# Optimization experiments

Measured on AMD Instinct MI355X. Metric: run time of the kernel, lower is better.

The kernel has to match this reference:

```python
import jax, jax.numpy as jnp
import numpy as np

B, S, D = 2, 2048, 2048
H, KV, HD = 32, 8, 64  # num_heads, num_kv_heads, head_dim
NREP = H // KV


def rotate_half(x):
    x1, x2 = x[..., : x.shape[-1] // 2], x[..., x.shape[-1] // 2 :]
    return jnp.concatenate((-x2, x1), axis=-1)


def setup_inputs() -> dict:
    key = jax.random.key(0)
    ks = jax.random.split(key, 5)
    x = jax.random.normal(ks[0], (B, S, D), dtype=jnp.float32)
    # weights stored as [in, out] so y = x @ W (same math as nn.Linear with random init)
    Wq = jax.random.normal(ks[1], (D, D), dtype=jnp.float32) * (D ** -0.5)
    Wk = jax.random.normal(ks[2], (D, KV * HD), dtype=jnp.float32) * (D ** -0.5)
    Wv = jax.random.normal(ks[3], (D, KV * HD), dtype=jnp.float32) * (D ** -0.5)
    Wo = jax.random.normal(ks[4], (D, D), dtype=jnp.float32) * (D ** -0.5)
    # standard RoPE tables, broadcastable over [B, H, S, HD]
    inv_freq = 1.0 / (10000.0 ** (jnp.arange(0, HD, 2, dtype=jnp.float32) / HD))
    freqs = jnp.arange(S, dtype=jnp.float32)[:, None] * inv_freq[None, :]  # [S, HD/2]
    emb = jnp.concatenate((freqs, freqs), axis=-1)  # [S, HD]
    cos = jnp.cos(emb)[None, None]  # [1,1,S,HD]
    sin = jnp.sin(emb)[None, None]
    # causal mask, masked where == 0
    attention_mask = jnp.tril(jnp.ones((S, S), dtype=jnp.int32))[None, None]
    return {"x": x, "cos": cos, "sin": sin, "Wq": Wq, "Wk": Wk, "Wv": Wv,
            "Wo": Wo, "attention_mask": attention_mask}


def reference(x, cos, sin, Wq, Wk, Wv, Wo, attention_mask):
    b, s, _ = x.shape
    q = (x @ Wq).reshape(b, s, H, HD).transpose(0, 2, 1, 3)   # [B,H,S,HD]
    k = (x @ Wk).reshape(b, s, KV, HD).transpose(0, 2, 1, 3)  # [B,KV,S,HD]
    v = (x @ Wv).reshape(b, s, KV, HD).transpose(0, 2, 1, 3)  # [B,KV,S,HD]
    # RoPE (elementwise) commutes with head-repeat; apply before grouping
    q = q * cos + rotate_half(q) * sin
    k = k * cos + rotate_half(k) * sin
    # GQA head broadcast instead of repeat_interleave: group q as [B,KV,NREP,S,HD]
    qg = q.reshape(b, KV, NREP, s, HD)
    scores = jnp.einsum('bgrqd,bgkd->bgrqk', qg, k) / jnp.sqrt(jnp.float32(HD))
    scores = jnp.where(attention_mask[:, :, None] == 0, jnp.float32(-1e9), scores)
    probs = jax.nn.softmax(scores, axis=-1)
    out = jnp.einsum('bgrqk,bgkd->bgrqd', probs, v)           # [B,KV,NREP,S,HD]
    out = out.reshape(b, H, s, HD).transpose(0, 2, 1, 3).reshape(b, s, H * HD)
    return out @ Wo
```

## Files before the change

### kernel.cpp

```cpp
#include <hip/hip_runtime.h>
#include <hip/hip_bf16.h>
#include <stdint.h>

#define B_ 2
#define S_ 2048
#define D_ 2048
#define H_ 32
#define KV_ 8
#define HD_ 64
#define NQKV 3072

typedef __bf16 bf16_t;
typedef __bf16 bf16x8 __attribute__((ext_vector_type(8)));
typedef __bf16 bf16x4 __attribute__((ext_vector_type(4)));
typedef float  f32x4  __attribute__((ext_vector_type(4)));
typedef float  f32x16 __attribute__((ext_vector_type(16)));
typedef unsigned int u32;
typedef u32 u32x4 __attribute__((ext_vector_type(4)));

typedef const __attribute__((address_space(1))) uint32_t* gp1_t;
typedef __attribute__((address_space(3))) uint32_t* lp3_t;

__device__ inline void gload_lds16(const void* g, void* l) {
  __builtin_amdgcn_global_load_lds((gp1_t)(uintptr_t)g, (lp3_t)(uint32_t)(uintptr_t)l,
                                   16, 0, 0);
}

__device__ inline u32 pkbf(float a, float b) {
  union { bf16_t h[2]; u32 u; } v;
  v.h[0] = (bf16_t)a; v.h[1] = (bf16_t)b;
  return v.u;
}

__device__ inline void pl32swap(u32 &a, u32 &b) {
  asm("v_permlane32_swap_b32 %0, %1" : "+v"(a), "+v"(b));
}

__global__ void cvt_f32_bf16(const float* __restrict__ in, bf16_t* __restrict__ out, int n4) {
  int i = blockIdx.x * blockDim.x + threadIdx.x;
  if (i < n4) {
    float4 v = ((const float4*)in)[i];
    bf16x4 o;
    o[0] = (bf16_t)v.x; o[1] = (bf16_t)v.y; o[2] = (bf16_t)v.z; o[3] = (bf16_t)v.w;
    ((bf16x4*)out)[i] = o;
  }
}

__global__ void transpose_cvt(const float* __restrict__ in, bf16_t* __restrict__ out,
                              int C, int row_off) {
  __shared__ float t[32][33];
  int tx = threadIdx.x, ty = threadIdx.y;
  int c0 = blockIdx.x * 32, r0 = blockIdx.y * 32;
#pragma unroll
  for (int j = 0; j < 4; ++j)
    t[ty + j*8][tx] = in[(int64_t)(r0 + ty + j*8) * C + c0 + tx];
  __syncthreads();
#pragma unroll
  for (int j = 0; j < 4; ++j)
    out[(int64_t)(row_off + c0 + ty + j*8) * 2048 + r0 + tx] = (bf16_t)t[tx][ty + j*8];
}

__global__ void v_transpose(const bf16_t* __restrict__ Vbuf, bf16_t* __restrict__ Vt) {
  __shared__ bf16_t t[32][34];
  const int tx = threadIdx.x, ty = threadIdx.y;
  const int c0 = blockIdx.x * 32;
  const int s0 = blockIdx.y * 32;
  const int b  = blockIdx.z;
#pragma unroll
  for (int j = 0; j < 4; ++j)
    t[ty + j*8][tx] = Vbuf[(int64_t)(b * S_ + s0 + ty + j*8) * 512 + c0 + tx];
  __syncthreads();
#pragma unroll
  for (int j = 0; j < 4; ++j)
    Vt[(int64_t)(b * 512 + c0 + ty + j*8) * S_ + s0 + tx] = t[tx][ty + j*8];
}

#define QSCALE 0.18033688011112042f
template <int BN, int EPI>
__global__ __launch_bounds__(512, 2) void gemm256(const bf16_t* __restrict__ A,
                                                  const bf16_t* __restrict__ Bt,
                                                  const float* __restrict__ cosb,
                                                  const float* __restrict__ sinb,
                                                  bf16_t* __restrict__ Q,
                                                  bf16_t* __restrict__ Kr,
                                                  bf16_t* __restrict__ Vbuf,
                                                  float* __restrict__ Cout,
                                                  int N, int K) {
  constexpr int NB = BN / 64;
  constexpr int LT = 4 + NB;
  constexpr int WCOLS = BN / 4;
  constexpr int NF = WCOLS / 16;

  __shared__ bf16_t As[2][256 * 64];
  __shared__ bf16_t Bs[2][BN * 64];

  const int tid = threadIdx.x;
  const int w = tid >> 6, lane = tid & 63;
  const int l15 = lane & 15, l4 = lane >> 4;
  const int wr = w >> 2, wc = w & 3;
  const int bm = blockIdx.y * 256, bn = blockIdx.x * BN;

  const int rw = w * 8 + (lane >> 3);
  const int srcg = ((lane & 7) ^ ((lane >> 3) & 7)) << 3;
  const bf16_t* PA[4];
  const bf16_t* PB[NB];
#pragma unroll
  for (int L = 0; L < 4; ++L)
    PA[L] = A + (int64_t)(bm + L * 64 + rw) * K + srcg;
#pragma unroll
  for (int L = 0; L < NB; ++L)
    PB[L] = Bt + (int64_t)(bn + L * 64 + rw) * K + srcg;

  const int NK = K >> 6;
  const int xr = l15 & 7;
  const int g0 = (l4 ^ xr) << 3;
  const int g1 = ((4 + l4) ^ xr) << 3;

  f32x4 acc[8][NF] = {};

#pragma unroll
  for (int s = 0; s < LT; ++s) {
    if (s < 4) gload_lds16(PA[s], &As[0][s * 4096 + w * 512]);
    else       gload_lds16(PB[s - 4], &Bs[0][(s - 4) * 4096 + w * 512]);
  }
  asm volatile("s_waitcnt vmcnt(0)" ::: "memory");
  __syncthreads();

  for (int t = 0; t < NK; ++t) {
    const int p = t & 1;
    const bool more = (t + 1) < NK;
    const int toff = (t + 1) << 6;
    const bf16_t* Ab = &As[p][0];
    const bf16_t* Bb = &Bs[p][0];

    bf16x8 ball[NF][2];
#pragma unroll
    for (int nn = 0; nn < NF; ++nn) {
      const int rb = wc * WCOLS + nn * 16 + l15;
      ball[nn][0] = *(const bf16x8*)(Bb + rb * 64 + g0);
      ball[nn][1] = *(const bf16x8*)(Bb + rb * 64 + g1);
    }

#pragma unroll
    for (int mh = 0; mh < 2; ++mh) {
      if (more) {
        const int s0 = mh * (LT / 2), s1 = s0 + LT / 2;
#pragma unroll
        for (int s = s0; s < s1; ++s) {
          if (s < 4) gload_lds16(PA[s] + toff, &As[p ^ 1][s * 4096 + w * 512]);
          else       gload_lds16(PB[s - 4] + toff, &Bs[p ^ 1][(s - 4) * 4096 + w * 512]);
        }
      }
      bf16x8 af[4][2];
#pragma unroll
      for (int mm = 0; mm < 4; ++mm) {
        const int ra = wr * 128 + (mh * 4 + mm) * 16 + l15;
        af[mm][0] = *(const bf16x8*)(Ab + ra * 64 + g0);
        af[mm][1] = *(const bf16x8*)(Ab + ra * 64 + g1);
      }
      __builtin_amdgcn_s_setprio(1);
#pragma unroll
      for (int mm = 0; mm < 4; ++mm)
#pragma unroll
        for (int nn = 0; nn < NF; ++nn) {
          acc[mh*4+mm][nn] = __builtin_amdgcn_mfma_f32_16x16x32_bf16(
              af[mm][0], ball[nn][0], acc[mh*4+mm][nn], 0, 0, 0);
          acc[mh*4+mm][nn] = __builtin_amdgcn_mfma_f32_16x16x32_bf16(
              af[mm][1], ball[nn][1], acc[mh*4+mm][nn], 0, 0, 0);
        }
      __builtin_amdgcn_s_setprio(0);
    }
    if (more) {
      asm volatile("s_waitcnt vmcnt(0)" ::: "memory");
      __syncthreads();
    }
  }

  if constexpr (EPI == 0) {
#pragma unroll
    for (int m = 0; m < 8; ++m) {
      const int row = bm + wr * 128 + m * 16 + l4 * 4;
#pragma unroll
      for (int n = 0; n < NF; ++n) {
        const int col = bn + wc * WCOLS + n * 16 + l15;
#pragma unroll
        for (int r = 0; r < 4; ++r)
          Cout[(int64_t)(row + r) * N + col] = acc[m][n][r];
      }
    }
  } else {
    const int colbase = bn + wc * 64;
    if (colbase < 2048) {
      const int h = colbase >> 6;
#pragma unroll
      for (int m = 0; m < 8; ++m) {
#pragma unroll
        for (int r = 0; r < 4; ++r) {
          const int srow = bm + wr * 128 + m * 16 + l4 * 4 + r;
          const int b = srow >> 11, s = srow & 2047;
          const float* cs = cosb + s * HD_;
          const float* sn = sinb + s * HD_;
          bf16_t* qp = Q + ((int64_t)(b * H_ + h) * S_ + s) * HD_;
#pragma unroll
          for (int n = 0; n < 4; ++n) {
            const int d = n * 16 + l15;
            const float sgn = (n & 2) ? 1.f : -1.f;
            float o = (acc[m][n][r] * cs[d] + sgn * acc[m][n ^ 2][r] * sn[d]) * QSCALE;
            qp[d] = (bf16_t)o;
          }
        }
      }
    } else if (colbase < 2560) {
      const int kvh = (colbase - 2048) >> 6;
#pragma unroll
      for (int m = 0; m < 8; ++m) {
#pragma unroll
        for (int r = 0; r < 4; ++r) {
          const int srow = bm + wr * 128 + m * 16 + l4 * 4 + r;
          const int b = srow >> 11, s = srow & 2047;
          const float* cs = cosb + s * HD_;
          const float* sn = sinb + s * HD_;
          bf16_t* kp = Kr + ((int64_t)(b * KV_ + kvh) * S_ + s) * HD_;
#pragma unroll
          for (int n = 0; n < 4; ++n) {
            const int d = n * 16 + l15;
            const float sgn = (n & 2) ? 1.f : -1.f;
            float o = acc[m][n][r] * cs[d] + sgn * acc[m][n ^ 2][r] * sn[d];
            kp[d] = (bf16_t)o;
          }
        }
      }
    } else {
      const int ccb = colbase - 2560;
#pragma unroll
      for (int m = 0; m < 8; ++m) {
#pragma unroll
        for (int r = 0; r < 4; ++r) {
          const int srow = bm + wr * 128 + m * 16 + l4 * 4 + r;
          bf16_t* vp = Vbuf + (int64_t)srow * 512 + ccb;
#pragma unroll
          for (int n = 0; n < 4; ++n)
            vp[n * 16 + l15] = (bf16_t)acc[m][n][r];
        }
      }
    }
  }
}

#define SHIFT_ 8.0f
__global__ __launch_bounds__(256, 2) void attn7(const bf16_t* __restrict__ Q,
                                                const bf16_t* __restrict__ Kr,
                                                const bf16_t* __restrict__ Vt,
                                                bf16_t* __restrict__ AO) {
  const int bk = blockIdx.x;
  const int b = bk >> 3, kvh = bk & 7;
  const int y = blockIdx.y;
  const int q0A = y * 32, q0B = (63 - y) * 32;
  const int tid = threadIdx.x;
  const int w = tid >> 6, lane = tid & 63;
  const int l31 = lane & 31, hi = lane >> 5;
  const int h = kvh * 4 + w;

  __shared__ __align__(16) bf16_t Ks[3][64 * 64];
  __shared__ __align__(16) bf16_t Vs[3][64 * 64];

  const bf16_t* Kg = Kr + (int64_t)(b * KV_ + kvh) * S_ * HD_;
  const bf16_t* Vg = Vt + (int64_t)(b * KV_ + kvh) * HD_ * S_;

  const int rL = (w << 3) + (lane >> 3);
  const int sgr = ((lane & 7) ^ (rL & 7)) << 3;
  const bf16_t* Ksrc = Kg + (int64_t)rL * HD_ + sgr;
  const bf16_t* Vsrc = Vg + (int64_t)rL * S_ + sgr;

  const int NT = (63 - y) / 2 + 1;

  auto stage = [&](int t) {
    const int tc = (t < NT) ? t : (NT - 1);
    char* Kd = (char*)Ks + (t % 3) * 8192 + w * 1024;
    char* Vd = (char*)Vs + (t % 3) * 8192 + w * 1024;
    gload_lds16(Ksrc + (int64_t)tc * 64 * HD_, Kd);
    gload_lds16(Ksrc + (int64_t)(tc * 64 + 32) * HD_, Kd + 4096);
    gload_lds16(Vsrc + tc * 64, Vd);
    gload_lds16(Vsrc + (int64_t)32 * S_ + tc * 64, Vd + 4096);
  };

  const bf16_t* QbA = Q + ((int64_t)(b * H_ + h) * S_ + q0A) * HD_;
  const bf16_t* QbB = Q + ((int64_t)(b * H_ + h) * S_ + q0B) * HD_;
  bf16x8 qfA[4], qfB[4];
#pragma unroll
  for (int ds = 0; ds < 4; ++ds) {
    qfA[ds] = *(const bf16x8*)(QbA + l31 * HD_ + ds * 16 + hi * 8);
    qfB[ds] = *(const bf16x8*)(QbB + l31 * HD_ + ds * 16 + hi * 8);
  }

  f32x16 aA0 = {}, aA1 = {}, aB0 = {}, aB1 = {};
  float lhA = 0.f, lhB = 0.f;
  const int xorb = l31 & 7;

  const f32x16 sinit = {-SHIFT_, -SHIFT_, -SHIFT_, -SHIFT_,
                        -SHIFT_, -SHIFT_, -SHIFT_, -SHIFT_,
                        -SHIFT_, -SHIFT_, -SHIFT_, -SHIFT_,
                        -SHIFT_, -SHIFT_, -SHIFT_, -SHIFT_};

  auto softmax_pack = [&](const f32x16 &sacc, bool diag, float &lh,
                          bf16x8 &pf0, bf16x8 &pf1) {
    float p[16];
#pragma unroll
    for (int r = 0; r < 16; ++r) {
      float sc = sacc[r];
      if (diag) {
        int kvpos = (r & 3) + 8 * (r >> 2) + 4 * hi;
        if (kvpos > l31) sc = -1e30f;
      }
      p[r] = __builtin_amdgcn_exp2f(sc);
    }
    float t0 = (p[0] + p[1]) + (p[2] + p[3]);
    float t1 = (p[4] + p[5]) + (p[6] + p[7]);
    float t2 = (p[8] + p[9]) + (p[10] + p[11]);
    float t3 = (p[12] + p[13]) + (p[14] + p[15]);
    lh += (t0 + t1) + (t2 + t3);
    u32 pk[8];
#pragma unroll
    for (int i = 0; i < 8; ++i) pk[i] = pkbf(p[2*i], p[2*i+1]);
    u32 a0 = pk[0], b0 = pk[2]; pl32swap(a0, b0);
    u32 a1 = pk[1], b1 = pk[3]; pl32swap(a1, b1);
    u32 a2 = pk[4], b2 = pk[6]; pl32swap(a2, b2);
    u32 a3 = pk[5], b3 = pk[7]; pl32swap(a3, b3);
    pf0 = __builtin_bit_cast(bf16x8, (u32x4){a0, a1, b0, b1});
    pf1 = __builtin_bit_cast(bf16x8, (u32x4){a2, a3, b2, b3});
  };

  stage(0);
  stage(1);

  for (int t = 0; t < NT; ++t) {
    asm volatile("s_waitcnt vmcnt(4)" ::: "memory");
    __syncthreads();
    stage(t + 2);
    const char* KsB = (const char*)Ks + (t % 3) * 8192;
    const char* VsB = (const char*)Vs + (t % 3) * 8192;
#pragma unroll
    for (int sub = 0; sub < 2; ++sub) {
      const int kvbase = t * 64 + sub * 32;
      if (kvbase <= q0B) {
        const bool actA = (kvbase <= q0A);
        const char* Kbase = KsB + (sub * 32 + l31) * 128;
        bf16x8 kf[4];
#pragma unroll
        for (int ds = 0; ds < 4; ++ds)
          kf[ds] = *(const bf16x8*)(Kbase + ((((ds << 1) + hi) ^ xorb) << 4));
        f32x16 sA = sinit, sB = sinit;
        __builtin_amdgcn_s_setprio(1);
#pragma unroll
        for (int ds = 0; ds < 4; ++ds)
          sB = __builtin_amdgcn_mfma_f32_32x32x16_bf16(kf[ds], qfB[ds], sB, 0, 0, 0);
        if (actA) {
#pragma unroll
          for (int ds = 0; ds < 4; ++ds)
            sA = __builtin_amdgcn_mfma_f32_32x32x16_bf16(kf[ds], qfA[ds], sA, 0, 0, 0);
        }
        __builtin_amdgcn_s_setprio(0);
        bf16x8 pA0, pA1, pB0, pB1;
        softmax_pack(sB, kvbase == q0B, lhB, pB0, pB1);
        if (actA) softmax_pack(sA, kvbase == q0A, lhA, pA0, pA1);
        const char* Vb0 = VsB + l31 * 128;
        const char* Vb1 = VsB + (32 + l31) * 128;
        const int c0 = (sub << 2) + hi;
        const int c1 = c0 + 2;
        bf16x8 v00 = *(const bf16x8*)(Vb0 + ((c0 ^ xorb) << 4));
        bf16x8 v01 = *(const bf16x8*)(Vb0 + ((c1 ^ xorb) << 4));
        bf16x8 v10 = *(const bf16x8*)(Vb1 + ((c0 ^ xorb) << 4));
        bf16x8 v11 = *(const bf16x8*)(Vb1 + ((c1 ^ xorb) << 4));
        __builtin_amdgcn_s_setprio(1);
        aB0 = __builtin_amdgcn_mfma_f32_32x32x16_bf16(v00, pB0, aB0, 0, 0, 0);
        aB1 = __builtin_amdgcn_mfma_f32_32x32x16_bf16(v10, pB0, aB1, 0, 0, 0);
        aB0 = __builtin_amdgcn_mfma_f32_32x32x16_bf16(v01, pB1, aB0, 0, 0, 0);
        aB1 = __builtin_amdgcn_mfma_f32_32x32x16_bf16(v11, pB1, aB1, 0, 0, 0);
        if (actA) {
          aA0 = __builtin_amdgcn_mfma_f32_32x32x16_bf16(v00, pA0, aA0, 0, 0, 0);
          aA1 = __builtin_amdgcn_mfma_f32_32x32x16_bf16(v10, pA0, aA1, 0, 0, 0);
          aA0 = __builtin_amdgcn_mfma_f32_32x32x16_bf16(v01, pA1, aA0, 0, 0, 0);
          aA1 = __builtin_amdgcn_mfma_f32_32x32x16_bf16(v11, pA1, aA1, 0, 0, 0);
        }
        __builtin_amdgcn_s_setprio(0);
      }
    }
  }

  asm volatile("s_waitcnt vmcnt(0)" ::: "memory");

  auto epi = [&](const f32x16 &a0, const f32x16 &a1, float lh, int q0) {
    float l = lh + __shfl_xor(lh, 32);
    const float rl = 1.f / l;
    const int64_t row = (int64_t)(b * S_ + q0 + l31);
#pragma unroll
    for (int dt = 0; dt < 2; ++dt) {
#pragma unroll
      for (int g = 0; g < 4; ++g) {
        bf16x4 ov;
#pragma unroll
        for (int j = 0; j < 4; ++j) {
          float val = (dt ? a1[4*g + j] : a0[4*g + j]) * rl;
          ov[j] = (bf16_t)val;
        }
        const int d0 = dt * 32 + g * 8 + hi * 4;
        *(bf16x4*)(AO + row * D_ + h * HD_ + d0) = ov;
      }
    }
  };
  epi(aA0, aA1, lhA, q0A);
  epi(aB0, aB1, lhB, q0B);
}

extern "C" void kernel_launch(void* const* d_in, const int* in_sizes, int n_in,
                              void* d_out, int out_size, void* d_ws, size_t ws_size,
                              hipStream_t stream) {
  const float* x    = (const float*)d_in[0];
  const float* cosb = (const float*)d_in[1];
  const float* sinb = (const float*)d_in[2];
  const float* Wq   = (const float*)d_in[3];
  const float* Wk   = (const float*)d_in[4];
  const float* Wv   = (const float*)d_in[5];
  const float* Wo   = (const float*)d_in[6];
  float* out = (float*)d_out;

  bf16_t* ws = (bf16_t*)d_ws;
  size_t o = 0;
  bf16_t* xb    = ws + o; o += (size_t)4096 * 2048;
  bf16_t* Wqkvt = ws + o; o += (size_t)3072 * 2048;
  bf16_t* Wot   = ws + o; o += (size_t)2048 * 2048;
  bf16_t* Qr    = ws + o; o += (size_t)B_ * H_ * S_ * HD_;
  bf16_t* Krb   = ws + o; o += (size_t)B_ * KV_ * S_ * HD_;
  bf16_t* Vtb   = ws + o; o += (size_t)B_ * KV_ * S_ * HD_;
  bf16_t* Vbuf  = ws + o; o += (size_t)B_ * S_ * 512;
  bf16_t* AO    = ws + o; o += (size_t)4096 * 2048;

  cvt_f32_bf16<<<(8388608/4 + 255)/256, 256, 0, stream>>>(x, xb, 8388608/4);
  transpose_cvt<<<dim3(2048/32, 2048/32), dim3(32, 8), 0, stream>>>(Wq, Wqkvt, 2048, 0);
  transpose_cvt<<<dim3(512/32, 2048/32),  dim3(32, 8), 0, stream>>>(Wk, Wqkvt, 512, 2048);
  transpose_cvt<<<dim3(512/32, 2048/32),  dim3(32, 8), 0, stream>>>(Wv, Wqkvt, 512, 2560);
  transpose_cvt<<<dim3(2048/32, 2048/32), dim3(32, 8), 0, stream>>>(Wo, Wot, 2048, 0);
  gemm256<256, 1><<<dim3(3072/256, 4096/256), 512, 0, stream>>>(
      xb, Wqkvt, cosb, sinb, Qr, Krb, Vbuf, nullptr, 3072, 2048);
  v_transpose<<<dim3(16, 64, 2), dim3(32, 8), 0, stream>>>(Vbuf, Vtb);
  attn7<<<dim3(16, 32), 256, 0, stream>>>(Qr, Krb, Vtb, AO);
  gemm256<128, 0><<<dim3(2048/128, 4096/256), 512, 0, stream>>>(
      AO, Wot, nullptr, nullptr, nullptr, nullptr, nullptr, out, 2048, 2048);
}
```

Baseline: 180.4 us.

## Restructure GEMM main loop into quadrant-phased schedule with explicit barriers

Splits each K-step of the bf16 MFMA GEMM into four quadrant phases (A-half × B-half). LDS fragment loads, async global-to-LDS prefetch and MFMA bursts are interleaved with s_barrier and lgkmcnt waits, in the style of an 8-wave ping-pong schedule. The aim is to overlap LDS reads and global prefetch with matrix work and to keep waves in lockstep. Register use drops because only half of B is loaded at a time. The risks are extra barrier stalls and lost compiler scheduling freedom from the sched_barrier calls.

Result: slower. 190.5 us (+5.6%).

```diff
diff --git a/kernel.cpp b/kernel.cpp
--- a/kernel.cpp
+++ b/kernel.cpp
@@ -77,19 +77,21 @@
 
 #define QSCALE 0.18033688011112042f
 template <int BN, int EPI>
-__global__ __launch_bounds__(512, 2) void gemm256(const bf16_t* __restrict__ A,
-                                                  const bf16_t* __restrict__ Bt,
-                                                  const float* __restrict__ cosb,
-                                                  const float* __restrict__ sinb,
-                                                  bf16_t* __restrict__ Q,
-                                                  bf16_t* __restrict__ Kr,
-                                                  bf16_t* __restrict__ Vbuf,
-                                                  float* __restrict__ Cout,
-                                                  int N, int K) {
+__global__ __launch_bounds__(512, 2) void gemm8p(const bf16_t* __restrict__ A,
+                                                 const bf16_t* __restrict__ Bt,
+                                                 const float* __restrict__ cosb,
+                                                 const float* __restrict__ sinb,
+                                                 bf16_t* __restrict__ Q,
+                                                 bf16_t* __restrict__ Kr,
+                                                 bf16_t* __restrict__ Vbuf,
+                                                 float* __restrict__ Cout,
+                                                 int N, int K) {
   constexpr int NB = BN / 64;
   constexpr int LT = 4 + NB;
+  constexpr int L0 = LT / 2;
   constexpr int WCOLS = BN / 4;
   constexpr int NF = WCOLS / 16;
+  constexpr int NH = NF / 2;
 
   __shared__ bf16_t As[2][256 * 64];
   __shared__ bf16_t Bs[2][BN * 64];
@@ -117,12 +119,49 @@
   const int g1 = ((4 + l4) ^ xr) << 3;
 
   f32x4 acc[8][NF] = {};
-
-#pragma unroll
-  for (int s = 0; s < LT; ++s) {
-    if (s < 4) gload_lds16(PA[s], &As[0][s * 4096 + w * 512]);
-    else       gload_lds16(PB[s - 4], &Bs[0][(s - 4) * 4096 + w * 512]);
-  }
+  bf16x8 aH[4][2];
+  bf16x8 bAll[NF][2];
+
+  auto stage = [&](int s, int buf, int toff) {
+    if (s < 4) gload_lds16(PA[s] + toff, &As[buf][s * 4096 + w * 512]);
+    else       gload_lds16(PB[s - 4] + toff, &Bs[buf][(s - 4) * 4096 + w * 512]);
+  };
+  auto ldA = [&](const bf16_t* Ab, int mh) {
+#pragma unroll
+    for (int mm = 0; mm < 4; ++mm) {
+      const int ra = wr * 128 + (mh * 4 + mm) * 16 + l15;
+      aH[mm][0] = *(const bf16x8*)(Ab + ra * 64 + g0);
+      aH[mm][1] = *(const bf16x8*)(Ab + ra * 64 + g1);
+    }
+  };
+  auto ldB = [&](const bf16_t* Bb, int nh) {
+#pragma unroll
+    for (int nn = 0; nn < NH; ++nn) {
+      const int rb = wc * WCOLS + (nh * NH + nn) * 16 + l15;
+      bAll[nh * NH + nn][0] = *(const bf16x8*)(Bb + rb * 64 + g0);
+      bAll[nh * NH + nn][1] = *(const bf16x8*)(Bb + rb * 64 + g1);
+    }
+  };
+  auto mfma_quad = [&](int mh, int nh) {
+    __builtin_amdgcn_s_setprio(1);
+#pragma unroll
+    for (int mm = 0; mm < 4; ++mm)
+#pragma unroll
+      for (int nn = 0; nn < NH; ++nn) {
+        acc[mh*4+mm][nh*NH+nn] = __builtin_amdgcn_mfma_f32_16x16x32_bf16(
+            aH[mm][0], bAll[nh*NH+nn][0], acc[mh*4+mm][nh*NH+nn], 0, 0, 0);
+        acc[mh*4+mm][nh*NH+nn] = __builtin_amdgcn_mfma_f32_16x16x32_bf16(
+            aH[mm][1], bAll[nh*NH+nn][1], acc[mh*4+mm][nh*NH+nn], 0, 0, 0);
+      }
+    __builtin_amdgcn_s_setprio(0);
+  };
+  auto wait_lds = [&]() {
+    asm volatile("s_waitcnt lgkmcnt(0)" ::: "memory");
+    __builtin_amdgcn_sched_barrier(0);
+  };
+
+#pragma unroll
+  for (int s = 0; s < LT; ++s) stage(s, 0, 0);
   asm volatile("s_waitcnt vmcnt(0)" ::: "memory");
   __syncthreads();
 
@@ -133,47 +172,38 @@
     const bf16_t* Ab = &As[p][0];
     const bf16_t* Bb = &Bs[p][0];
 
-    bf16x8 ball[NF][2];
-#pragma unroll
-    for (int nn = 0; nn < NF; ++nn) {
-      const int rb = wc * WCOLS + nn * 16 + l15;
-      ball[nn][0] = *(const bf16x8*)(Bb + rb * 64 + g0);
-      ball[nn][1] = *(const bf16x8*)(Bb + rb * 64 + g1);
-    }
-
-#pragma unroll
-    for (int mh = 0; mh < 2; ++mh) {
-      if (more) {
-        const int s0 = mh * (LT / 2), s1 = s0 + LT / 2;
-#pragma unroll
-        for (int s = s0; s < s1; ++s) {
-          if (s < 4) gload_lds16(PA[s] + toff, &As[p ^ 1][s * 4096 + w * 512]);
-          else       gload_lds16(PB[s - 4] + toff, &Bs[p ^ 1][(s - 4) * 4096 + w * 512]);
-        }
-      }
-      bf16x8 af[4][2];
-#pragma unroll
-      for (int mm = 0; mm < 4; ++mm) {
-        const int ra = wr * 128 + (mh * 4 + mm) * 16 + l15;
-        af[mm][0] = *(const bf16x8*)(Ab + ra * 64 + g0);
-        af[mm][1] = *(const bf16x8*)(Ab + ra * 64 + g1);
-      }
-      __builtin_amdgcn_s_setprio(1);
-#pragma unroll
-      for (int mm = 0; mm < 4; ++mm)
-#pragma unroll
-        for (int nn = 0; nn < NF; ++nn) {
-          acc[mh*4+mm][nn] = __builtin_amdgcn_mfma_f32_16x16x32_bf16(
-              af[mm][0], ball[nn][0], acc[mh*4+mm][nn], 0, 0, 0);
-          acc[mh*4+mm][nn] = __builtin_amdgcn_mfma_f32_16x16x32_bf16(
-              af[mm][1], ball[nn][1], acc[mh*4+mm][nn], 0, 0, 0);
-        }
-      __builtin_amdgcn_s_setprio(0);
-    }
+    ldA(Ab, 0);
+    ldB(Bb, 0);
+    if (more) {
+#pragma unroll
+      for (int s = 0; s < L0; ++s) stage(s, p ^ 1, toff);
+    }
+    __builtin_amdgcn_s_barrier();
+    wait_lds();
+    mfma_quad(0, 0);
+    __builtin_amdgcn_s_barrier();
+
+    ldB(Bb, 1);
+    if (more) {
+#pragma unroll
+      for (int s = L0; s < LT; ++s) stage(s, p ^ 1, toff);
+    }
+    __builtin_amdgcn_s_barrier();
+    wait_lds();
+    mfma_quad(0, 1);
+    __builtin_amdgcn_s_barrier();
+
+    ldA(Ab, 1);
+    __builtin_amdgcn_s_barrier();
+    wait_lds();
+    mfma_quad(1, 1);
+    __builtin_amdgcn_s_barrier();
+
+    mfma_quad(1, 0);
     if (more) {
       asm volatile("s_waitcnt vmcnt(0)" ::: "memory");
-      __syncthreads();
-    }
+    }
+    __builtin_amdgcn_s_barrier();
   }
 
   if constexpr (EPI == 0) {
@@ -440,10 +470,10 @@
   transpose_cvt<<<dim3(512/32, 2048/32),  dim3(32, 8), 0, stream>>>(Wk, Wqkvt, 512, 2048);
   transpose_cvt<<<dim3(512/32, 2048/32),  dim3(32, 8), 0, stream>>>(Wv, Wqkvt, 512, 2560);
   transpose_cvt<<<dim3(2048/32, 2048/32), dim3(32, 8), 0, stream>>>(Wo, Wot, 2048, 0);
-  gemm256<256, 1><<<dim3(3072/256, 4096/256), 512, 0, stream>>>(
+  gemm8p<256, 1><<<dim3(3072/256, 4096/256), 512, 0, stream>>>(
       xb, Wqkvt, cosb, sinb, Qr, Krb, Vbuf, nullptr, 3072, 2048);
   v_transpose<<<dim3(16, 64, 2), dim3(32, 8), 0, stream>>>(Vbuf, Vtb);
   attn7<<<dim3(16, 32), 256, 0, stream>>>(Qr, Krb, Vtb, AO);
-  gemm256<128, 0><<<dim3(2048/128, 4096/256), 512, 0, stream>>>(
+  gemm8p<128, 0><<<dim3(2048/128, 4096/256), 512, 0, stream>>>(
       AO, Wot, nullptr, nullptr, nullptr, nullptr, nullptr, out, 2048, 2048);
 }
```

## Restructure GEMM mainloop into 4-buffer K=32 pipeline with counted vmcnt waits

Applied to the files above, without the earlier changes.

The GEMM mainloop drops the two-buffer K=64 scheme, where each step drained all loads with vmcnt(0) before a full barrier. It now uses four LDS buffers of K=32 slices with loads issued two stages ahead and a partial vmcnt wait. This lets global-to-LDS loads for later stages stay in flight while the current slice is computed, aiming to hide memory latency. In exchange it issues more, smaller stages with more barriers and less MFMA work per barrier. The tail clamps prefetch indices to the last slice, so redundant loads are issued at the end.

After: 188.0 us. 4.2% more time.

```diff
diff --git a/kernel.cpp b/kernel.cpp
--- a/kernel.cpp
+++ b/kernel.cpp
@@ -77,22 +77,22 @@
 
 #define QSCALE 0.18033688011112042f
 template <int BN, int EPI>
-__global__ __launch_bounds__(512, 2) void gemm256(const bf16_t* __restrict__ A,
-                                                  const bf16_t* __restrict__ Bt,
-                                                  const float* __restrict__ cosb,
-                                                  const float* __restrict__ sinb,
-                                                  bf16_t* __restrict__ Q,
-                                                  bf16_t* __restrict__ Kr,
-                                                  bf16_t* __restrict__ Vbuf,
-                                                  float* __restrict__ Cout,
-                                                  int N, int K) {
-  constexpr int NB = BN / 64;
-  constexpr int LT = 4 + NB;
+__global__ __launch_bounds__(512, 2) void gemm_cnt(const bf16_t* __restrict__ A,
+                                                   const bf16_t* __restrict__ Bt,
+                                                   const float* __restrict__ cosb,
+                                                   const float* __restrict__ sinb,
+                                                   bf16_t* __restrict__ Q,
+                                                   bf16_t* __restrict__ Kr,
+                                                   bf16_t* __restrict__ Vbuf,
+                                                   float* __restrict__ Cout,
+                                                   int N, int K) {
+  constexpr int NBC = BN / 128;
+  constexpr int LT = 2 + NBC;
   constexpr int WCOLS = BN / 4;
   constexpr int NF = WCOLS / 16;
 
-  __shared__ bf16_t As[2][256 * 64];
-  __shared__ bf16_t Bs[2][BN * 64];
+  __shared__ bf16_t As[4][256 * 32];
+  __shared__ bf16_t Bs[4][BN * 32];
 
   const int tid = threadIdx.x;
   const int w = tid >> 6, lane = tid & 63;
@@ -100,81 +100,78 @@
   const int wr = w >> 2, wc = w & 3;
   const int bm = blockIdx.y * 256, bn = blockIdx.x * BN;
 
-  const int rw = w * 8 + (lane >> 3);
-  const int srcg = ((lane & 7) ^ ((lane >> 3) & 7)) << 3;
-  const bf16_t* PA[4];
-  const bf16_t* PB[NB];
-#pragma unroll
-  for (int L = 0; L < 4; ++L)
-    PA[L] = A + (int64_t)(bm + L * 64 + rw) * K + srcg;
-#pragma unroll
-  for (int L = 0; L < NB; ++L)
-    PB[L] = Bt + (int64_t)(bn + L * 64 + rw) * K + srcg;
-
-  const int NK = K >> 6;
-  const int xr = l15 & 7;
-  const int g0 = (l4 ^ xr) << 3;
-  const int g1 = ((4 + l4) ^ xr) << 3;
+  const int rw = w * 16 + (lane >> 2);
+  const int srcg = ((lane & 3) ^ ((lane >> 2) & 3)) << 3;
+  const bf16_t* PA[2];
+  const bf16_t* PB[NBC];
+#pragma unroll
+  for (int c = 0; c < 2; ++c)
+    PA[c] = A + (int64_t)(bm + c * 128 + rw) * K + srcg;
+#pragma unroll
+  for (int c = 0; c < NBC; ++c)
+    PB[c] = Bt + (int64_t)(bn + c * 128 + rw) * K + srcg;
+
+  const int NS = K >> 5;
+  const int gg = ((l4 ^ (l15 & 3)) << 4);
 
   f32x4 acc[8][NF] = {};
 
-#pragma unroll
-  for (int s = 0; s < LT; ++s) {
-    if (s < 4) gload_lds16(PA[s], &As[0][s * 4096 + w * 512]);
-    else       gload_lds16(PB[s - 4], &Bs[0][(s - 4) * 4096 + w * 512]);
+  auto stage = [&](int s, int buf) {
+    const int off = s << 5;
+#pragma unroll
+    for (int c = 0; c < 2; ++c)
+      gload_lds16(PA[c] + off, (char*)&As[buf][0] + c * 8192 + w * 1024);
+#pragma unroll
+    for (int c = 0; c < NBC; ++c)
+      gload_lds16(PB[c] + off, (char*)&Bs[buf][0] + c * 8192 + w * 1024);
+  };
+
+  auto wait_cnt = [&]() {
+    if constexpr (LT == 4) asm volatile("s_waitcnt vmcnt(4)" ::: "memory");
+    else                   asm volatile("s_waitcnt vmcnt(3)" ::: "memory");
+    asm volatile("s_barrier" ::: "memory");
+  };
+
+  auto compute = [&](int buf) {
+    const char* Ab = (const char*)&As[buf][0];
+    const char* Bb = (const char*)&Bs[buf][0];
+    bf16x8 bfv[NF];
+#pragma unroll
+    for (int nn = 0; nn < NF; ++nn) {
+      const int rb = wc * WCOLS + nn * 16 + l15;
+      bfv[nn] = *(const bf16x8*)(Bb + rb * 64 + gg);
+    }
+    bf16x8 af[8];
+#pragma unroll
+    for (int mm = 0; mm < 8; ++mm) {
+      const int ra = wr * 128 + mm * 16 + l15;
+      af[mm] = *(const bf16x8*)(Ab + ra * 64 + gg);
+    }
+    __builtin_amdgcn_s_setprio(1);
+#pragma unroll
+    for (int mm = 0; mm < 8; ++mm)
+#pragma unroll
+      for (int nn = 0; nn < NF; ++nn)
+        acc[mm][nn] = __builtin_amdgcn_mfma_f32_16x16x32_bf16(
+            af[mm], bfv[nn], acc[mm][nn], 0, 0, 0);
+    __builtin_amdgcn_s_setprio(0);
+  };
+
+  stage(0, 0);
+  stage(1, 1);
+  wait_cnt();
+
+  for (int s0 = 0; s0 < NS; s0 += 4) {
+#pragma unroll
+    for (int u = 0; u < 4; ++u) {
+      const int s = s0 + u;
+      const int t2 = (s + 2 < NS) ? (s + 2) : (NS - 1);
+      stage(t2, (u + 2) & 3);
+      compute(u);
+      wait_cnt();
+    }
   }
   asm volatile("s_waitcnt vmcnt(0)" ::: "memory");
-  __syncthreads();
-
-  for (int t = 0; t < NK; ++t) {
-    const int p = t & 1;
-    const bool more = (t + 1) < NK;
-    const int toff = (t + 1) << 6;
-    const bf16_t* Ab = &As[p][0];
-    const bf16_t* Bb = &Bs[p][0];
-
-    bf16x8 ball[NF][2];
-#pragma unroll
-    for (int nn = 0; nn < NF; ++nn) {
-      const int rb = wc * WCOLS + nn * 16 + l15;
-      ball[nn][0] = *(const bf16x8*)(Bb + rb * 64 + g0);
-      ball[nn][1] = *(const bf16x8*)(Bb + rb * 64 + g1);
-    }
-
-#pragma unroll
-    for (int mh = 0; mh < 2; ++mh) {
-      if (more) {
-        const int s0 = mh * (LT / 2), s1 = s0 + LT / 2;
-#pragma unroll
-        for (int s = s0; s < s1; ++s) {
-          if (s < 4) gload_lds16(PA[s] + toff, &As[p ^ 1][s * 4096 + w * 512]);
-          else       gload_lds16(PB[s - 4] + toff, &Bs[p ^ 1][(s - 4) * 4096 + w * 512]);
-        }
-      }
-      bf16x8 af[4][2];
-#pragma unroll
-      for (int mm = 0; mm < 4; ++mm) {
-        const int ra = wr * 128 + (mh * 4 + mm) * 16 + l15;
-        af[mm][0] = *(const bf16x8*)(Ab + ra * 64 + g0);
-        af[mm][1] = *(const bf16x8*)(Ab + ra * 64 + g1);
-      }
-      __builtin_amdgcn_s_setprio(1);
-#pragma unroll
-      for (int mm = 0; mm < 4; ++mm)
-#pragma unroll
-        for (int nn = 0; nn < NF; ++nn) {
-          acc[mh*4+mm][nn] = __builtin_amdgcn_mfma_f32_16x16x32_bf16(
-              af[mm][0], ball[nn][0], acc[mh*4+mm][nn], 0, 0, 0);
-          acc[mh*4+mm][nn] = __builtin_amdgcn_mfma_f32_16x16x32_bf16(
-              af[mm][1], ball[nn][1], acc[mh*4+mm][nn], 0, 0, 0);
-        }
-      __builtin_amdgcn_s_setprio(0);
-    }
-    if (more) {
-      asm volatile("s_waitcnt vmcnt(0)" ::: "memory");
-      __syncthreads();
-    }
-  }
 
   if constexpr (EPI == 0) {
 #pragma unroll
@@ -440,10 +437,10 @@
   transpose_cvt<<<dim3(512/32, 2048/32),  dim3(32, 8), 0, stream>>>(Wk, Wqkvt, 512, 2048);
   transpose_cvt<<<dim3(512/32, 2048/32),  dim3(32, 8), 0, stream>>>(Wv, Wqkvt, 512, 2560);
   transpose_cvt<<<dim3(2048/32, 2048/32), dim3(32, 8), 0, stream>>>(Wo, Wot, 2048, 0);
-  gemm256<256, 1><<<dim3(3072/256, 4096/256), 512, 0, stream>>>(
+  gemm_cnt<256, 1><<<dim3(3072/256, 4096/256), 512, 0, stream>>>(
       xb, Wqkvt, cosb, sinb, Qr, Krb, Vbuf, nullptr, 3072, 2048);
   v_transpose<<<dim3(16, 64, 2), dim3(32, 8), 0, stream>>>(Vbuf, Vtb);
   attn7<<<dim3(16, 32), 256, 0, stream>>>(Qr, Krb, Vtb, AO);
-  gemm256<128, 0><<<dim3(2048/128, 4096/256), 512, 0, stream>>>(
+  gemm_cnt<128, 0><<<dim3(2048/128, 4096/256), 512, 0, stream>>>(
       AO, Wot, nullptr, nullptr, nullptr, nullptr, nullptr, out, 2048, 2048);
 }
```

## Unfuse RoPE from QKV GEMM and use 192-wide tiles for full CU coverage

Applied to the files above, without the earlier changes.

The QKV projection GEMM now writes a plain bf16 [4096,3072] qkv buffer using a 192-column tile, which gives 256 blocks instead of 192 to fill more CUs. RoPE and the Q/K head scatter move into a separate vectorized rope_scatter2 kernel, and v_transpose reads V directly from the qkv buffer. The epilogue of the templated GEMM is simplified to a generic store with an output type parameter. In exchange this adds an extra kernel launch and a full round-trip of the qkv intermediate through memory.

Measured after the change: 180.2 us. About the same (-0.1%).

```diff
diff --git a/kernel.cpp b/kernel.cpp
--- a/kernel.cpp
+++ b/kernel.cpp
@@ -60,7 +60,7 @@
     out[(int64_t)(row_off + c0 + ty + j*8) * 2048 + r0 + tx] = (bf16_t)t[tx][ty + j*8];
 }
 
-__global__ void v_transpose(const bf16_t* __restrict__ Vbuf, bf16_t* __restrict__ Vt) {
+__global__ void v_transpose(const bf16_t* __restrict__ qkv, bf16_t* __restrict__ Vt) {
   __shared__ bf16_t t[32][34];
   const int tx = threadIdx.x, ty = threadIdx.y;
   const int c0 = blockIdx.x * 32;
@@ -68,7 +68,7 @@
   const int b  = blockIdx.z;
 #pragma unroll
   for (int j = 0; j < 4; ++j)
-    t[ty + j*8][tx] = Vbuf[(int64_t)(b * S_ + s0 + ty + j*8) * 512 + c0 + tx];
+    t[ty + j*8][tx] = qkv[(int64_t)(b * S_ + s0 + ty + j*8) * NQKV + 2560 + c0 + tx];
   __syncthreads();
 #pragma unroll
   for (int j = 0; j < 4; ++j)
@@ -76,15 +76,53 @@
 }
 
 #define QSCALE 0.18033688011112042f
-template <int BN, int EPI>
+__global__ __launch_bounds__(256) void rope_scatter2(const bf16_t* __restrict__ qkv,
+                                                     const float* __restrict__ cosb,
+                                                     const float* __restrict__ sinb,
+                                                     bf16_t* __restrict__ Q,
+                                                     bf16_t* __restrict__ Kr) {
+  const int row = blockIdx.x;
+  const int b = row >> 11, s = row & 2047;
+  const bf16_t* src = qkv + (int64_t)row * NQKV;
+  const float* cs = cosb + s * HD_;
+  const float* sn = sinb + s * HD_;
+  const int tid = threadIdx.x;
+  {
+    const int c0 = tid * 8;
+    const int d0 = c0 & 63, h = c0 >> 6;
+    bf16x8 own = *(const bf16x8*)(src + c0);
+    bf16x8 par = *(const bf16x8*)(src + (c0 ^ 32));
+    const float sgn = (d0 & 32) ? 1.f : -1.f;
+    bf16x8 o;
+#pragma unroll
+    for (int j = 0; j < 8; ++j) {
+      const int d = d0 + j;
+      float val = (float)own[j] * cs[d] + sgn * (float)par[j] * sn[d];
+      o[j] = (bf16_t)(val * QSCALE);
+    }
+    *(bf16x8*)(Q + ((int64_t)(b * H_ + h) * S_ + s) * HD_ + d0) = o;
+  }
+  if (tid < 64) {
+    const int c0 = 2048 + tid * 8;
+    const int d0 = (tid * 8) & 63, kvh = tid >> 3;
+    bf16x8 own = *(const bf16x8*)(src + c0);
+    bf16x8 par = *(const bf16x8*)(src + (c0 ^ 32));
+    const float sgn = (d0 & 32) ? 1.f : -1.f;
+    bf16x8 o;
+#pragma unroll
+    for (int j = 0; j < 8; ++j) {
+      const int d = d0 + j;
+      float val = (float)own[j] * cs[d] + sgn * (float)par[j] * sn[d];
+      o[j] = (bf16_t)val;
+    }
+    *(bf16x8*)(Kr + ((int64_t)(b * KV_ + kvh) * S_ + s) * HD_ + d0) = o;
+  }
+}
+
+template <int BN, int EPI, typename OutT>
 __global__ __launch_bounds__(512, 2) void gemm256(const bf16_t* __restrict__ A,
                                                   const bf16_t* __restrict__ Bt,
-                                                  const float* __restrict__ cosb,
-                                                  const float* __restrict__ sinb,
-                                                  bf16_t* __restrict__ Q,
-                                                  bf16_t* __restrict__ Kr,
-                                                  bf16_t* __restrict__ Vbuf,
-                                                  float* __restrict__ Cout,
+                                                  OutT* __restrict__ Cout,
                                                   int N, int K) {
   constexpr int NB = BN / 64;
   constexpr int LT = 4 + NB;
@@ -118,11 +156,13 @@
 
   f32x4 acc[8][NF] = {};
 
-#pragma unroll
-  for (int s = 0; s < LT; ++s) {
-    if (s < 4) gload_lds16(PA[s], &As[0][s * 4096 + w * 512]);
-    else       gload_lds16(PB[s - 4], &Bs[0][(s - 4) * 4096 + w * 512]);
-  }
+  auto stage = [&](int s, int buf, int toff) {
+    if (s < 4) gload_lds16(PA[s] + toff, &As[buf][s * 4096 + w * 512]);
+    else       gload_lds16(PB[s - 4] + toff, &Bs[buf][(s - 4) * 4096 + w * 512]);
+  };
+
+#pragma unroll
+  for (int s = 0; s < LT; ++s) stage(s, 0, 0);
   asm volatile("s_waitcnt vmcnt(0)" ::: "memory");
   __syncthreads();
 
@@ -144,12 +184,10 @@
 #pragma unroll
     for (int mh = 0; mh < 2; ++mh) {
       if (more) {
-        const int s0 = mh * (LT / 2), s1 = s0 + LT / 2;
-#pragma unroll
-        for (int s = s0; s < s1; ++s) {
-          if (s < 4) gload_lds16(PA[s] + toff, &As[p ^ 1][s * 4096 + w * 512]);
-          else       gload_lds16(PB[s - 4] + toff, &Bs[p ^ 1][(s - 4) * 4096 + w * 512]);
-        }
+        const int sb = mh * (LT / 2);
+        const int se = (mh == 0) ? (LT / 2) : LT;
+#pragma unroll
+        for (int s = sb; s < se; ++s) stage(s, p ^ 1, toff);
       }
       bf16x8 af[4][2];
 #pragma unroll
@@ -176,73 +214,15 @@
     }
   }
 
-  if constexpr (EPI == 0) {
-#pragma unroll
-    for (int m = 0; m < 8; ++m) {
-      const int row = bm + wr * 128 + m * 16 + l4 * 4;
-#pragma unroll
-      for (int n = 0; n < NF; ++n) {
-        const int col = bn + wc * WCOLS + n * 16 + l15;
-#pragma unroll
-        for (int r = 0; r < 4; ++r)
-          Cout[(int64_t)(row + r) * N + col] = acc[m][n][r];
-      }
-    }
-  } else {
-    const int colbase = bn + wc * 64;
-    if (colbase < 2048) {
-      const int h = colbase >> 6;
-#pragma unroll
-      for (int m = 0; m < 8; ++m) {
-#pragma unroll
-        for (int r = 0; r < 4; ++r) {
-          const int srow = bm + wr * 128 + m * 16 + l4 * 4 + r;
-          const int b = srow >> 11, s = srow & 2047;
-          const float* cs = cosb + s * HD_;
-          const float* sn = sinb + s * HD_;
-          bf16_t* qp = Q + ((int64_t)(b * H_ + h) * S_ + s) * HD_;
-#pragma unroll
-          for (int n = 0; n < 4; ++n) {
-            const int d = n * 16 + l15;
-            const float sgn = (n & 2) ? 1.f : -1.f;
-            float o = (acc[m][n][r] * cs[d] + sgn * acc[m][n ^ 2][r] * sn[d]) * QSCALE;
-            qp[d] = (bf16_t)o;
-          }
-        }
-      }
-    } else if (colbase < 2560) {
-      const int kvh = (colbase - 2048) >> 6;
-#pragma unroll
-      for (int m = 0; m < 8; ++m) {
-#pragma unroll
-        for (int r = 0; r < 4; ++r) {
-          const int srow = bm + wr * 128 + m * 16 + l4 * 4 + r;
-          const int b = srow >> 11, s = srow & 2047;
-          const float* cs = cosb + s * HD_;
-          const float* sn = sinb + s * HD_;
-          bf16_t* kp = Kr + ((int64_t)(b * KV_ + kvh) * S_ + s) * HD_;
-#pragma unroll
-          for (int n = 0; n < 4; ++n) {
-            const int d = n * 16 + l15;
-            const float sgn = (n & 2) ? 1.f : -1.f;
-            float o = acc[m][n][r] * cs[d] + sgn * acc[m][n ^ 2][r] * sn[d];
-            kp[d] = (bf16_t)o;
-          }
-        }
-      }
-    } else {
-      const int ccb = colbase - 2560;
-#pragma unroll
-      for (int m = 0; m < 8; ++m) {
-#pragma unroll
-        for (int r = 0; r < 4; ++r) {
-          const int srow = bm + wr * 128 + m * 16 + l4 * 4 + r;
-          bf16_t* vp = Vbuf + (int64_t)srow * 512 + ccb;
-#pragma unroll
-          for (int n = 0; n < 4; ++n)
-            vp[n * 16 + l15] = (bf16_t)acc[m][n][r];
-        }
-      }
+#pragma unroll
+  for (int m = 0; m < 8; ++m) {
+    const int row = bm + wr * 128 + m * 16 + l4 * 4;
+#pragma unroll
+    for (int n = 0; n < NF; ++n) {
+      const int col = bn + wc * WCOLS + n * 16 + l15;
+#pragma unroll
+      for (int r = 0; r < 4; ++r)
+        Cout[(int64_t)(row + r) * N + col] = (OutT)acc[m][n][r];
     }
   }
 }
@@ -429,10 +409,10 @@
   bf16_t* xb    = ws + o; o += (size_t)4096 * 2048;
   bf16_t* Wqkvt = ws + o; o += (size_t)3072 * 2048;
   bf16_t* Wot   = ws + o; o += (size_t)2048 * 2048;
+  bf16_t* qkv   = ws + o; o += (size_t)4096 * 3072;
   bf16_t* Qr    = ws + o; o += (size_t)B_ * H_ * S_ * HD_;
   bf16_t* Krb   = ws + o; o += (size_t)B_ * KV_ * S_ * HD_;
   bf16_t* Vtb   = ws + o; o += (size_t)B_ * KV_ * S_ * HD_;
-  bf16_t* Vbuf  = ws + o; o += (size_t)B_ * S_ * 512;
   bf16_t* AO    = ws + o; o += (size_t)4096 * 2048;
 
   cvt_f32_bf16<<<(8388608/4 + 255)/256, 256, 0, stream>>>(x, xb, 8388608/4);
@@ -440,10 +420,11 @@
   transpose_cvt<<<dim3(512/32, 2048/32),  dim3(32, 8), 0, stream>>>(Wk, Wqkvt, 512, 2048);
   transpose_cvt<<<dim3(512/32, 2048/32),  dim3(32, 8), 0, stream>>>(Wv, Wqkvt, 512, 2560);
   transpose_cvt<<<dim3(2048/32, 2048/32), dim3(32, 8), 0, stream>>>(Wo, Wot, 2048, 0);
-  gemm256<256, 1><<<dim3(3072/256, 4096/256), 512, 0, stream>>>(
-      xb, Wqkvt, cosb, sinb, Qr, Krb, Vbuf, nullptr, 3072, 2048);
-  v_transpose<<<dim3(16, 64, 2), dim3(32, 8), 0, stream>>>(Vbuf, Vtb);
+  gemm256<192, 2, bf16_t><<<dim3(3072/192, 4096/256), 512, 0, stream>>>(
+      xb, Wqkvt, qkv, 3072, 2048);
+  rope_scatter2<<<4096, 256, 0, stream>>>(qkv, cosb, sinb, Qr, Krb);
+  v_transpose<<<dim3(16, 64, 2), dim3(32, 8), 0, stream>>>(qkv, Vtb);
   attn7<<<dim3(16, 32), 256, 0, stream>>>(Qr, Krb, Vtb, AO);
-  gemm256<128, 0><<<dim3(2048/128, 4096/256), 512, 0, stream>>>(
-      AO, Wot, nullptr, nullptr, nullptr, nullptr, nullptr, out, 2048, 2048);
-}
+  gemm256<128, 0, float><<<dim3(2048/128, 4096/256), 512, 0, stream>>>(
+      AO, Wot, out, 2048, 2048);
+}
```
